# Performance work log

Hardware: AMD Instinct MI355X
Metric: run time of the kernel (lower is better)

The kernel has to match this reference:

```python
import jax, jax.numpy as jnp
import numpy as np

M, P, B = 64, 256, 4096  # blocks per row/col, block size, batch


def setup_inputs() -> dict:
    key = jax.random.key(0)
    ks = jax.random.split(key, 6)
    u = lambda k, shape: jax.random.uniform(k, shape, jnp.float32, -0.1, 0.1)
    return {
        "x": jax.random.normal(ks[0], (B, M * P), dtype=jnp.float32),
        "Wd": u(ks[1], (M, P, P)),      # diag blocks (nn.Linear weights)
        "Wu": u(ks[2], (M - 1, P, P)),  # upper off-diagonal blocks
        "Wl": u(ks[3], (M - 1, P, P)),  # lower off-diagonal blocks
        "Wtr": u(ks[4], (P, P)),        # top-right corner block (periodic)
        "Wbl": u(ks[5], (P, P)),        # bottom-left corner block (periodic)
    }


def reference(x, Wd, Wu, Wl, Wtr, Wbl):
    # BlockXDiag forward, diag_type='tri', periodic=True, transpose=False,
    # bias=False, activation=None (identity). nn.Linear: o = x @ W.T
    Bsz = x.shape[0]
    xb = x.reshape(Bsz, M, P)  # [B, M, P]
    # diagonal: result[:, i] = x_i @ Wd[i].T  -> batched over all M blocks
    out = jnp.einsum('bip,iqp->biq', xb, Wd)
    # upper band: result[:, i] += x_{i+1} @ Wu[i].T, i in [0, M-2]
    out = out.at[:, : M - 1].add(jnp.einsum('bip,iqp->biq', xb[:, 1:], Wu))
    # lower band: result[:, i] += x_{i-1} @ Wl[i-1].T, i in [1, M-1]
    out = out.at[:, 1:].add(jnp.einsum('bip,iqp->biq', xb[:, : M - 1], Wl))
    # periodic corners
    out = out.at[:, 0].add(xb[:, M - 1] @ Wtr.T)
    out = out.at[:, M - 1].add(xb[:, 0] @ Wbl.T)
    return out.reshape(Bsz, M * P)
```

## Files before the change

### kernel.cpp

```cpp
#include <hip/hip_runtime.h>


#define MB   64
#define PB   256
#define NPR  16384
#define BM   128
#define BN   128
#define BK   32
#define KTOT 768

typedef __bf16 bf16x8 __attribute__((ext_vector_type(8)));
typedef float  f32x4  __attribute__((ext_vector_type(4)));
typedef unsigned short u16x4 __attribute__((ext_vector_type(4)));

__device__ __forceinline__ unsigned short f2bf(float f) {
    unsigned u = __float_as_uint(f);
    u += 0x7fffu + ((u >> 16) & 1u);
    return (unsigned short)(u >> 16);
}

__global__ __launch_bounds__(256, 2)
void bxd_kernel(const float* __restrict__ x,
                const float* __restrict__ Wd,
                const float* __restrict__ Wu,
                const float* __restrict__ Wl,
                const float* __restrict__ Wtr,
                const float* __restrict__ Wbl,
                float* __restrict__ out)
{
    __shared__ unsigned short sA[BM * BK];
    __shared__ unsigned short sB[BN * BK];

    const int i  = blockIdx.x >> 1;
    const int nt = blockIdx.x & 1;
    const int mt = blockIdx.y;

    const int t    = threadIdx.x;
    const int lane = t & 63;
    const int wave = t >> 6;
    const int wm   = wave & 1;
    const int wn   = wave >> 1;
    const int quad = lane >> 4;
    const int l16  = lane & 15;

    const int srow = t >> 3;
    const int scol = (t & 7) * 4;

    const float* wptr[3];
    wptr[0] = (i == 0)      ? Wtr : (Wl + (size_t)(i - 1) * (PB * PB));
    wptr[1] = Wd + (size_t)i * (PB * PB);
    wptr[2] = (i == MB - 1) ? Wbl : (Wu + (size_t)i * (PB * PB));
    const int jblk[3] = { (i + MB - 1) & (MB - 1), i, (i + 1) & (MB - 1) };

    f32x4 acc[4][4];
    #pragma unroll
    for (int a = 0; a < 4; ++a)
        #pragma unroll
        for (int b = 0; b < 4; ++b)
            acc[a][b] = (f32x4){0.f, 0.f, 0.f, 0.f};

    for (int kt = 0; kt < KTOT / BK; ++kt) {
        const int c  = kt >> 3;
        const int kb = kt & 7;

        const float* aSrc = x + (size_t)(mt * BM + srow) * NPR
                              + jblk[c] * PB + kb * BK + scol;
        const float* bSrc = wptr[c] + (size_t)(nt * BN + srow) * PB
                              + kb * BK + scol;

        float4 av[4], bv[4];
        #pragma unroll
        for (int p = 0; p < 4; ++p) {
            av[p] = *(const float4*)(aSrc + (size_t)p * 32 * NPR);
            bv[p] = *(const float4*)(bSrc + (size_t)p * 32 * PB);
        }

        __syncthreads();
        #pragma unroll
        for (int p = 0; p < 4; ++p) {
            u16x4 ra = { f2bf(av[p].x), f2bf(av[p].y), f2bf(av[p].z), f2bf(av[p].w) };
            *(u16x4*)&sA[(srow + p * 32) * BK + scol] = ra;
            u16x4 rb = { f2bf(bv[p].x), f2bf(bv[p].y), f2bf(bv[p].z), f2bf(bv[p].w) };
            *(u16x4*)&sB[(srow + p * 32) * BK + scol] = rb;
        }
        __syncthreads();

        bf16x8 afrag[4], bfrag[4];
        #pragma unroll
        for (int mi = 0; mi < 4; ++mi)
            afrag[mi] = *(const bf16x8*)&sA[(wm * 64 + mi * 16 + l16) * BK + quad * 8];
        #pragma unroll
        for (int ni = 0; ni < 4; ++ni)
            bfrag[ni] = *(const bf16x8*)&sB[(wn * 64 + ni * 16 + l16) * BK + quad * 8];

        #pragma unroll
        for (int mi = 0; mi < 4; ++mi)
            #pragma unroll
            for (int ni = 0; ni < 4; ++ni)
                acc[mi][ni] = __builtin_amdgcn_mfma_f32_16x16x32_bf16(
                    afrag[mi], bfrag[ni], acc[mi][ni], 0, 0, 0);
    }

    const int colb = i * PB + nt * BN + wn * 64;
    #pragma unroll
    for (int mi = 0; mi < 4; ++mi) {
        #pragma unroll
        for (int ni = 0; ni < 4; ++ni) {
            #pragma unroll
            for (int r = 0; r < 4; ++r) {
                const int row = mt * BM + wm * 64 + mi * 16 + quad * 4 + r;
                out[(size_t)row * NPR + colb + ni * 16 + l16] = acc[mi][ni][r];
            }
        }
    }
}

extern "C" void kernel_launch(void* const* d_in, const int* in_sizes, int n_in,
                              void* d_out, int out_size, void* d_ws, size_t ws_size,
                              hipStream_t stream) {
    const float* x   = (const float*)d_in[0];
    const float* Wd  = (const float*)d_in[1];
    const float* Wu  = (const float*)d_in[2];
    const float* Wl  = (const float*)d_in[3];
    const float* Wtr = (const float*)d_in[4];
    const float* Wbl = (const float*)d_in[5];
    float* out = (float*)d_out;

    dim3 grid(MB * 2, 4096 / BM, 1);
    dim3 block(256, 1, 1);
    hipLaunchKernelGGL(bxd_kernel, grid, block, 0, stream,
                       x, Wd, Wu, Wl, Wtr, Wbl, out);
}
```

Before: 770.0 us.

## Pre-convert inputs to bf16 in workspace and load tiles directly into LDS

Adds two pre-pass kernels that convert x and the three weight bands (with the corner blocks folded in) to bf16 in the workspace. The GEMM kernel then uses global_load_lds to copy bf16 tiles straight into shared memory, skipping the per-tile fp32 loads and register conversion, and allows higher occupancy. This halves the bytes the GEMM reads for x and weights, which it fetches several times. In exchange it adds an extra full pass over x (fp32 read plus bf16 write). The new path runs only when the workspace is large enough; otherwise the old kernel is used.

```diff
diff --git a/kernel.cpp b/kernel.cpp
--- a/kernel.cpp
+++ b/kernel.cpp
@@ -4,6 +4,7 @@
 #define MB   64
 #define PB   256
 #define NPR  16384
+#define BSZ  4096
 #define BM   128
 #define BN   128
 #define BK   32
@@ -12,11 +13,128 @@
 typedef __bf16 bf16x8 __attribute__((ext_vector_type(8)));
 typedef float  f32x4  __attribute__((ext_vector_type(4)));
 typedef unsigned short u16x4 __attribute__((ext_vector_type(4)));
+typedef unsigned short u16x8 __attribute__((ext_vector_type(8)));
 
 __device__ __forceinline__ unsigned short f2bf(float f) {
     unsigned u = __float_as_uint(f);
     u += 0x7fffu + ((u >> 16) & 1u);
     return (unsigned short)(u >> 16);
+}
+
+__device__ __forceinline__ void gload_lds16(const void* g, void* l) {
+    __builtin_amdgcn_global_load_lds(
+        (const __attribute__((address_space(1))) void*)g,
+        (__attribute__((address_space(3))) void*)l, 16, 0, 0);
+}
+
+__global__ __launch_bounds__(256)
+void cvt_x(const float* __restrict__ in, __bf16* __restrict__ o, int n8) {
+    int idx    = blockIdx.x * 256 + threadIdx.x;
+    int stride = gridDim.x * 256;
+    for (; idx < n8; idx += stride) {
+        const float4* p = (const float4*)in + (size_t)idx * 2;
+        float4 a = p[0], b = p[1];
+        u16x8 r = { f2bf(a.x), f2bf(a.y), f2bf(a.z), f2bf(a.w),
+                    f2bf(b.x), f2bf(b.y), f2bf(b.z), f2bf(b.w) };
+        *((u16x8*)o + idx) = r;
+    }
+}
+
+__global__ __launch_bounds__(256)
+void cvt_w(const float* __restrict__ Wd, const float* __restrict__ Wu,
+           const float* __restrict__ Wl, const float* __restrict__ Wtr,
+           const float* __restrict__ Wbl, __bf16* __restrict__ wcat) {
+    const int i = blockIdx.y;
+    const int c = blockIdx.z;
+    const float* src;
+    if      (c == 0) src = (i == 0)      ? Wtr : Wl + (size_t)(i - 1) * (PB * PB);
+    else if (c == 1) src = Wd + (size_t)i * (PB * PB);
+    else             src = (i == MB - 1) ? Wbl : Wu + (size_t)i * (PB * PB);
+
+    const int off = (blockIdx.x * 256 + threadIdx.x) * 8;
+    const float4* p = (const float4*)(src + off);
+    float4 a = p[0], b = p[1];
+    u16x8 r = { f2bf(a.x), f2bf(a.y), f2bf(a.z), f2bf(a.w),
+                f2bf(b.x), f2bf(b.y), f2bf(b.z), f2bf(b.w) };
+    *(u16x8*)(wcat + (size_t)(i * 3 + c) * (PB * PB) + off) = r;
+}
+
+__global__ __launch_bounds__(256, 4)
+void bxd_bf16(const __bf16* __restrict__ xb, const __bf16* __restrict__ wcat,
+              float* __restrict__ out)
+{
+    __shared__ __bf16 sA[BM * BK];
+    __shared__ __bf16 sB[BN * BK];
+
+    const int i  = blockIdx.x >> 1;
+    const int nt = blockIdx.x & 1;
+    const int mt = blockIdx.y;
+
+    const int t    = threadIdx.x;
+    const int lane = t & 63;
+    const int wave = t >> 6;
+    const int wm   = wave & 1;
+    const int wn   = wave >> 1;
+    const int quad = lane >> 4;
+    const int l16  = lane & 15;
+
+    const int jblk[3] = { (i + MB - 1) & (MB - 1), i, (i + 1) & (MB - 1) };
+
+    const int row0 = t >> 2;
+    const int kc   = (t & 3) * 8;
+
+    f32x4 acc[4][4];
+    #pragma unroll
+    for (int a = 0; a < 4; ++a)
+        #pragma unroll
+        for (int b = 0; b < 4; ++b)
+            acc[a][b] = (f32x4){0.f, 0.f, 0.f, 0.f};
+
+    for (int kt = 0; kt < KTOT / BK; ++kt) {
+        const int c  = kt >> 3;
+        const int kb = kt & 7;
+
+        const __bf16* aBase = xb + (size_t)(mt * BM) * NPR + jblk[c] * PB + kb * BK;
+        const __bf16* bBase = wcat + (size_t)(i * 3 + c) * (PB * PB)
+                                   + (size_t)(nt * BN) * PB + kb * BK;
+
+        __syncthreads();
+        #pragma unroll
+        for (int p = 0; p < 2; ++p) {
+            const int r = row0 + p * 64;
+            gload_lds16(aBase + (size_t)r * NPR + kc, &sA[(t + p * 256) * 8]);
+            gload_lds16(bBase + (size_t)r * PB  + kc, &sB[(t + p * 256) * 8]);
+        }
+        __syncthreads();
+
+        bf16x8 afrag[4], bfrag[4];
+        #pragma unroll
+        for (int mi = 0; mi < 4; ++mi)
+            afrag[mi] = *(const bf16x8*)&sA[(wm * 64 + mi * 16 + l16) * BK + quad * 8];
+        #pragma unroll
+        for (int ni = 0; ni < 4; ++ni)
+            bfrag[ni] = *(const bf16x8*)&sB[(wn * 64 + ni * 16 + l16) * BK + quad * 8];
+
+        #pragma unroll
+        for (int mi = 0; mi < 4; ++mi)
+            #pragma unroll
+            for (int ni = 0; ni < 4; ++ni)
+                acc[mi][ni] = __builtin_amdgcn_mfma_f32_16x16x32_bf16(
+                    afrag[mi], bfrag[ni], acc[mi][ni], 0, 0, 0);
+    }
+
+    const int colb = i * PB + nt * BN + wn * 64;
+    #pragma unroll
+    for (int mi = 0; mi < 4; ++mi) {
+        #pragma unroll
+        for (int ni = 0; ni < 4; ++ni) {
+            #pragma unroll
+            for (int r = 0; r < 4; ++r) {
+                const int row = mt * BM + wm * 64 + mi * 16 + quad * 4 + r;
+                out[(size_t)row * NPR + colb + ni * 16 + l16] = acc[mi][ni][r];
+            }
+        }
+    }
 }
 
 __global__ __launch_bounds__(256, 2)
@@ -126,8 +244,22 @@
     const float* Wbl = (const float*)d_in[5];
     float* out = (float*)d_out;
 
-    dim3 grid(MB * 2, 4096 / BM, 1);
-    dim3 block(256, 1, 1);
-    hipLaunchKernelGGL(bxd_kernel, grid, block, 0, stream,
-                       x, Wd, Wu, Wl, Wtr, Wbl, out);
-}
+    const size_t xbytes = (size_t)BSZ * NPR * sizeof(__bf16);
+    const size_t wbytes = (size_t)MB * 3 * PB * PB * sizeof(__bf16);
+
+    if (ws_size >= xbytes + wbytes) {
+        __bf16* xbuf = (__bf16*)d_ws;
+        __bf16* wcat = (__bf16*)((char*)d_ws + xbytes);
+        hipLaunchKernelGGL(cvt_x, dim3(2048), dim3(256), 0, stream,
+                           x, xbuf, (int)((size_t)BSZ * NPR / 8));
+        hipLaunchKernelGGL(cvt_w, dim3(32, 64, 3), dim3(256), 0, stream,
+                           Wd, Wu, Wl, Wtr, Wbl, wcat);
+        hipLaunchKernelGGL(bxd_bf16, dim3(MB * 2, BSZ / BM), dim3(256), 0, stream,
+                           xbuf, wcat, out);
+    } else {
+        dim3 grid(MB * 2, BSZ / BM, 1);
+        dim3 block(256, 1, 1);
+        hipLaunchKernelGGL(bxd_kernel, grid, block, 0, stream,
+                           x, Wd, Wu, Wl, Wtr, Wbl, out);
+    }
+}
```

Measured after the change: 697.0 us. 9.5% less time.
